# Optimization experiments

Measured on AMD Instinct MI355X. Metric: run time of the kernel, lower is better.

Reference implementation:

```python
import jax, jax.numpy as jnp
import numpy as np

B = 32768
EPS = 0.2  # BatchNorm eps used in the original module


def _xavier(key, shape):
    fan_in, fan_out = shape[-2], shape[-1]
    std = (2.0 / (fan_in + fan_out)) ** 0.5
    return (jax.random.normal(key, shape, jnp.float32) * std).astype(jnp.float32)


def bn(x, g, b):
    # training-mode BatchNorm1d: batch stats over the batch axis (-2), biased var
    m = jnp.mean(x, axis=-2, keepdims=True)
    v = jnp.mean(jnp.square(x - m), axis=-2, keepdims=True)
    return (x - m) * jax.lax.rsqrt(v + EPS) * g + b


def setup_inputs() -> dict:
    key = jax.random.key(0)
    ks = iter(jax.random.split(key, 48))
    inp = {}
    inp['x1f'] = jax.random.normal(next(ks), (B, 512), jnp.float32)
    inp['x2f'] = jax.random.normal(next(ks), (B, 512), jnp.float32)
    # shared trunk
    inp['W1'] = _xavier(next(ks), (512, 256)); inp['b1'] = jnp.zeros(256, jnp.float32)
    inp['W2'] = _xavier(next(ks), (256, 256)); inp['b2'] = jnp.zeros(256, jnp.float32)
    # batchnorm affine params (bn1:256, bn2:256, bn3:128, bn4:64)
    inp['g1'] = jnp.ones(256, jnp.float32); inp['be1'] = jnp.zeros(256, jnp.float32)
    inp['g2'] = jnp.ones(256, jnp.float32); inp['be2'] = jnp.zeros(256, jnp.float32)
    inp['g3'] = jnp.ones(128, jnp.float32); inp['be3'] = jnp.zeros(128, jnp.float32)
    inp['g4'] = jnp.ones(64, jnp.float32); inp['be4'] = jnp.zeros(64, jnp.float32)
    # 4 branch projections from each stream (x11..x14, x21..x24), stacked on axis 0
    inp['Wbx1'] = _xavier(next(ks), (4, 256, 256)); inp['bbx1'] = jnp.zeros((4, 256), jnp.float32)
    inp['Wbx2'] = _xavier(next(ks), (4, 256, 256)); inp['bbx2'] = jnp.zeros((4, 256), jnp.float32)
    # gating MLPs (xw*1, xw*2, xw*3, y*), stacked over the 4 attributes
    inp['Wwa'] = _xavier(next(ks), (4, 512, 128)); inp['bwa'] = jnp.zeros((4, 128), jnp.float32)
    inp['Wwb'] = _xavier(next(ks), (4, 128, 64)); inp['bwb'] = jnp.zeros((4, 64), jnp.float32)
    inp['Wwc'] = _xavier(next(ks), (4, 64, 64)); inp['bwc'] = jnp.zeros((4, 64), jnp.float32)
    inp['Wy'] = _xavier(next(ks), (4, 64, 2)); inp['by'] = jnp.zeros((4, 2), jnp.float32)
    # combine layers x1c..x4c, stacked
    inp['Wc'] = _xavier(next(ks), (4, 512, 256)); inp['bc'] = jnp.zeros((4, 256), jnp.float32)
    # output heads (different class counts: 3, 3, 6, 4)
    inp['Wo1'] = _xavier(next(ks), (256, 3)); inp['bo1'] = jnp.zeros(3, jnp.float32)
    inp['Wo2'] = _xavier(next(ks), (256, 3)); inp['bo2'] = jnp.zeros(3, jnp.float32)
    inp['Wo3'] = _xavier(next(ks), (256, 6)); inp['bo3'] = jnp.zeros(6, jnp.float32)
    inp['Wo4'] = _xavier(next(ks), (256, 4)); inp['bo4'] = jnp.zeros(4, jnp.float32)
    return inp


def reference(x1f, x2f, W1, b1, W2, b2, g1, be1, g2, be2, g3, be3, g4, be4,
              Wbx1, bbx1, Wbx2, bbx2, Wwa, bwa, Wwb, bwb, Wwc, bwc, Wy, by,
              Wc, bc, Wo1, bo1, Wo2, bo2, Wo3, bo3, Wo4, bo4):
    relu = jax.nn.relu

    def trunk(x):
        h = bn(relu(x @ W1 + b1), g1, be1)
        return bn(relu(h @ W2 + b2), g2, be2)

    h1 = trunk(x1f)  # [B,256]
    h2 = trunk(x2f)  # [B,256]

    # 4 branch features per stream, each bn1-normalized: [4,B,256]
    b1x = bn(relu(jnp.einsum('bi,kio->kbo', h1, Wbx1) + bbx1[:, None, :]), g1, be1)
    b2x = bn(relu(jnp.einsum('bi,kio->kbo', h2, Wbx2) + bbx2[:, None, :]), g1, be1)

    # gating MLP per attribute -> 2-way softmax weights
    xcat = jnp.concatenate([b1x, b2x], axis=-1)  # [4,B,512]
    a = bn(relu(jnp.einsum('kbi,kio->kbo', xcat, Wwa) + bwa[:, None, :]), g3, be3)
    b_ = bn(relu(jnp.einsum('kbi,kio->kbo', a, Wwb) + bwb[:, None, :]), g4, be4)
    c = bn(relu(jnp.einsum('kbi,kio->kbo', b_, Wwc) + bwc[:, None, :]), g4, be4)
    y = jax.nn.softmax(jnp.einsum('kbi,kio->kbo', c, Wy) + by[:, None, :], axis=-1)  # [4,B,2]

    # the original per-column loop == one broadcast multiply per stream
    xw = jnp.concatenate([b1x * y[..., 0:1], b2x * y[..., 1:2]], axis=-1)  # [4,B,512]

    # combine layers (dropout is identity in eval)
    xc = bn(relu(jnp.einsum('kbi,kio->kbo', xw, Wc) + bc[:, None, :]), g1, be1)  # [4,B,256]

    y1o = jax.nn.softmax(xc[0] @ Wo1 + bo1, axis=-1)
    y2o = jax.nn.softmax(xc[1] @ Wo2 + bo2, axis=-1)
    y3o = jax.nn.softmax(xc[2] @ Wo3 + bo3, axis=-1)
    y4o = jax.nn.softmax(xc[3] @ Wo4 + bo4, axis=-1)
    return (y1o, y2o, y3o, y4o)
```

## Files before the change

### kernel.cpp

```cpp
#include <hip/hip_runtime.h>
#include <hip/hip_bf16.h>


typedef unsigned short u16;
typedef _Float16 f16x8 __attribute__((ext_vector_type(8)));
typedef float f32x4 __attribute__((ext_vector_type(4)));

#define B_ROWS 32768
#define EPS_BN 0.2f
#define BINV (1.0f / 32768.0f)

__device__ __forceinline__ float bf2f(u16 u) {
    union { unsigned int i; float f; } c;
    c.i = ((unsigned int)u) << 16;
    return c.f;
}
__device__ __forceinline__ u16 f2bf(float f) {
    union { float f; unsigned int i; } c;
    c.f = f;
    unsigned int x = c.i;
    return (u16)((x + 0x7FFFu + ((x >> 16) & 1u)) >> 16);
}
__device__ __forceinline__ float h2f(u16 u) {
    _Float16 h;
    __builtin_memcpy(&h, &u, 2);
    return (float)h;
}
__device__ __forceinline__ u16 f2h(float f) {
    _Float16 h = (_Float16)f;
    u16 u;
    __builtin_memcpy(&u, &h, 2);
    return u;
}
__device__ __forceinline__ float ldp(const void* p, long i, int flag) {
    return flag ? bf2f(((const u16*)p)[i]) : ((const float*)p)[i];
}
__device__ __forceinline__ void gload16(const u16* gp, u16* lp) {
    __builtin_amdgcn_global_load_lds(
        (const __attribute__((address_space(1))) unsigned int*)gp,
        (__attribute__((address_space(3))) unsigned int*)lp, 16, 0, 0);
}

__global__ void detect_dtype(const u16* __restrict__ x, int* __restrict__ flag) {
    const int lane = threadIdx.x;
    const u16 v = x[2 * lane];
    const int e = (v >> 7) & 0xFF;
    const bool plausible = (e >= 110 && e <= 140);
    const unsigned long long m = __ballot(plausible);
    if (lane == 0) *flag = (__popcll(m) >= 58) ? 1 : 0;
}

struct PTab { const void* p[20]; int n[20]; int off[20]; };

__global__ void convert_params(PTab t, float* __restrict__ dst,
                               const int* __restrict__ flag) {
    const int ti = blockIdx.y;
    const int n = t.n[ti];
    float* o = dst + t.off[ti];
    const int isbf = *flag;
    for (int i = blockIdx.x * 256 + threadIdx.x; i < n; i += gridDim.x * 256)
        o[i] = ldp(t.p[ti], i, isbf);
}

__global__ __launch_bounds__(256) void prep_w(
    const void* __restrict__ W, long wstride,
    const void* __restrict__ bias, long bstride,
    const float* __restrict__ psum, const float* __restrict__ psq, int pstride,
    const void* __restrict__ pg, const void* __restrict__ pbe, int gmask,
    const int* __restrict__ dtflag,
    u16* __restrict__ Wt, long wtstride,
    float* __restrict__ biasP, float* __restrict__ T0o,
    float* __restrict__ T1o, float* __restrict__ bsum, long bost,
    int K, int khalf)
{
    const int tid = threadIdx.x;
    const int n = blockIdx.x;
    const int N = gridDim.x;
    const int inst = blockIdx.y;
    const int flag = *dtflag;
    __shared__ float sn[512], tn[512];
    __shared__ float r0[4], r1[4];

    for (int i = tid; i < K; i += 256) {
        float s = 1.f, t = 0.f;
        if (psum) {
            float m = psum[(long)pstride * inst + i] * BINV;
            float v = psq[(long)pstride * inst + i] * BINV - m * m;
            float g = ldp(pg, i & gmask, flag);
            float b = ldp(pbe, i & gmask, flag);
            s = g * rsqrtf(v + EPS_BN);
            t = b - m * s;
        }
        sn[i] = s; tn[i] = t;
    }
    __syncthreads();
    float p0 = 0.f, p1 = 0.f;
    for (int k = tid; k < K; k += 256) {
        float wv = ldp(W, wstride * inst + (long)k * N + n, flag);
        Wt[wtstride * inst + (long)n * K + k] = f2h(sn[k] * wv);
        float tw = tn[k] * wv;
        if (k < khalf) p0 += tw; else p1 += tw;
    }
#pragma unroll
    for (int off = 32; off; off >>= 1) {
        p0 += __shfl_xor(p0, off);
        p1 += __shfl_xor(p1, off);
    }
    const int lane = tid & 63, wid = tid >> 6;
    if (lane == 0) { r0[wid] = p0; r1[wid] = p1; }
    __syncthreads();
    if (tid == 0) {
        float t0 = r0[0] + r0[1] + r0[2] + r0[3];
        float t1 = r1[0] + r1[1] + r1[2] + r1[3];
        float bp = ldp(bias, bstride * inst + n, flag);
        long o = bost * inst + n;
        biasP[o] = bp; T0o[o] = t0; T1o[o] = t1; bsum[o] = bp + t0 + t1;
    }
}

__global__ __launch_bounds__(256) void reduce_stats(
    const float* __restrict__ part, int X, int colsPer,
    float* __restrict__ outS, float* __restrict__ outQ, int total)
{
    const int t = blockIdx.x * 256 + threadIdx.x;
    if (t >= total) return;
    const int p = t / colsPer, c = t % colsPer;
    const float* pb = part + (long)p * X * 2 * colsPer + c;
    float s = 0.f, q = 0.f;
#pragma unroll 4
    for (int x = 0; x < X; ++x) {
        s += pb[(long)x * 2 * colsPer];
        q += pb[(long)x * 2 * colsPer + colsPer];
    }
    outS[t] = s; outQ[t] = q;
}

template <bool XSTAGE, bool ROWW, int WM, int WN, int K, int RMODE>
__global__ __launch_bounds__(256, 3) void gemm_mfma(
    const void* __restrict__ X, const void* __restrict__ X2,
    long xstride, int ximask, int ldx, int ksplit, long ksecond,
    const int* __restrict__ dtflag,
    const u16* __restrict__ Wt, long wtstride,
    const float* __restrict__ biasP, const float* __restrict__ T0,
    const float* __restrict__ T1, const float* __restrict__ bsum, int bN,
    u16* __restrict__ Out, long ostride, int ldout,
    float* __restrict__ gsum, float* __restrict__ gsq, int sstride,
    float* __restrict__ part,
    const float* __restrict__ Y0v)
{
    const int tid = threadIdx.x;
    const int lane = tid & 63;
    const int wid = tid >> 6;
    const int wm = wid / WN, wn = wid % WN;

    const int gx = gridDim.x, gy = gridDim.y;
    const int NB = gx * gy * gridDim.z;
    const int L = blockIdx.x + gx * (blockIdx.y + gy * blockIdx.z);
    const int lid = (NB % 8 == 0) ? (L % 8) * (NB / 8) + L / 8 : L;
    int bx, by, inst;
    if constexpr (RMODE == 0) {
        bx = lid % gx; const int r = lid / gx; by = r % gy; inst = r / gy;
    } else if constexpr (RMODE == 1) {
        const int grp = gy * gridDim.z;
        bx = lid / grp; const int r = lid % grp; by = r % gy; inst = r / gy;
    } else {
        by = lid % gy; const int r = lid / gy; bx = r % gx; inst = r / gx;
    }

    const int rowB = bx * (64 * WM);
    const int nBase = by * (64 * WN);
    const int n0 = nBase + wn * 64;
    const int fm = lane & 15, quad = lane >> 4;

    __shared__ __align__(16) u16 AsBs[(WM + WN) * 4096];
    __shared__ float redS[4][64];
    __shared__ float redQ[4][64];
    u16* As = AsBs;
    u16* Bs = AsBs + WM * 4096;

    bool xf32 = false;
    if constexpr (XSTAGE) xf32 = (*dtflag == 0);
    const char* xb;
    if (XSTAGE) xb = (const char*)(inst == 0 ? X : X2);
    else        xb = (const char*)X + 2l * xstride * (inst & ximask);
    const u16* wtp = Wt + wtstride * inst;
    u16* op = Out + ostride * inst;

    f32x4 acc[4][4];
#pragma unroll
    for (int i = 0; i < 4; ++i)
#pragma unroll
        for (int j = 0; j < 4; ++j) acc[i][j] = (f32x4){0.f, 0.f, 0.f, 0.f};

    _Float16 ysc[2][4];
    if constexpr (ROWW) {
        const float* yp = Y0v + (long)inst * B_ROWS;
#pragma unroll
        for (int mi = 0; mi < 4; ++mi) {
            const float y = yp[rowB + wm * 64 + mi * 16 + fm];
            ysc[0][mi] = (_Float16)y;
            ysc[1][mi] = (_Float16)(1.f - y);
        }
    }

    const int rloc = lane >> 3;
    const int cg = (lane & 7) ^ rloc;

    for (int kt = 0; kt < K / 64; ++kt) {
        const int kk = kt * 64;
        __syncthreads();
        if constexpr (XSTAGE) {
#pragma unroll
            for (int p = 0; p < WM * 2; ++p) {
                const int s = p * 256 + tid;
                const int m = s >> 3, c = s & 7;
                const int g = c ^ (m & 7);
                f16x8 h;
                if (xf32) {
                    const float* gp = (const float*)xb + (long)(rowB + m) * ldx + kk + g * 8;
                    const float4 u = *(const float4*)gp;
                    const float4 u2 = *(const float4*)(gp + 4);
                    h[0] = (_Float16)u.x;  h[1] = (_Float16)u.y;
                    h[2] = (_Float16)u.z;  h[3] = (_Float16)u.w;
                    h[4] = (_Float16)u2.x; h[5] = (_Float16)u2.y;
                    h[6] = (_Float16)u2.z; h[7] = (_Float16)u2.w;
                } else {
                    const uint4 v = *(const uint4*)((const u16*)xb + (long)(rowB + m) * ldx + kk + g * 8);
                    const u16* pv = (const u16*)&v;
#pragma unroll
                    for (int j = 0; j < 8; ++j) h[j] = (_Float16)bf2f(pv[j]);
                }
                *(f16x8*)&As[s * 8] = h;
            }
        } else {
            const u16* xs = (const u16*)xb;
            int kkr = kk;
            if (kk >= ksplit) { xs += ksecond; kkr -= ksplit; }
#pragma unroll
            for (int s = wid; s < WM * 8; s += 4)
                gload16(xs + (long)(rowB + s * 8 + rloc) * ldx + kkr + cg * 8,
                        &As[s * 512 + lane * 8]);
        }
#pragma unroll
        for (int s = wid; s < WN * 8; s += 4)
            gload16(wtp + (long)(nBase + s * 8 + rloc) * K + kk + cg * 8,
                    &Bs[s * 512 + lane * 8]);
        __syncthreads();

        const int sel = (ROWW && kk >= ksplit) ? 1 : 0;
#pragma unroll
        for (int q = 0; q < 2; ++q) {
            f16x8 af[4], bfr[4];
#pragma unroll
            for (int mi = 0; mi < 4; ++mi) {
                const int mm = wm * 64 + mi * 16 + fm;
                af[mi] = *(const f16x8*)&As[mm * 64 + (((q * 4 + quad) ^ (mm & 7)) * 8)];
            }
            if constexpr (ROWW) {
#pragma unroll
                for (int mi = 0; mi < 4; ++mi) {
                    const _Float16 yh = ysc[sel][mi];
#pragma unroll
                    for (int j = 0; j < 8; ++j) af[mi][j] *= yh;
                }
            }
#pragma unroll
            for (int ni = 0; ni < 4; ++ni) {
                const int nn = wn * 64 + ni * 16 + fm;
                bfr[ni] = *(const f16x8*)&Bs[nn * 64 + (((q * 4 + quad) ^ (nn & 7)) * 8)];
            }
#pragma unroll
            for (int mi = 0; mi < 4; ++mi)
#pragma unroll
                for (int ni = 0; ni < 4; ++ni)
                    acc[mi][ni] = __builtin_amdgcn_mfma_f32_16x16x32_f16(
                        af[mi], bfr[ni], acc[mi][ni], 0, 0, 0);
        }
    }

    __syncthreads();

    u16* wtile = AsBs + wid * 4096;
    const int R0 = rowB + wm * 64;

    float yv[16];
    if constexpr (ROWW) {
        const float* yp = Y0v + (long)inst * B_ROWS;
#pragma unroll
        for (int mi = 0; mi < 4; ++mi)
#pragma unroll
            for (int r = 0; r < 4; ++r)
                yv[mi * 4 + r] = yp[R0 + mi * 16 + quad * 4 + r];
    }

#pragma unroll
    for (int ni = 0; ni < 4; ++ni) {
        const int nc = ni * 16 + fm;
        const int n = n0 + nc;
        float bS = 0.f, bP = 0.f, t0v = 0.f, t1v = 0.f;
        if constexpr (ROWW) {
            bP = biasP[(long)inst * bN + n];
            t0v = T0[(long)inst * bN + n];
            t1v = T1[(long)inst * bN + n];
        } else {
            bS = bsum[(long)inst * bN + n];
        }
        float s = 0.f, qq = 0.f;
#pragma unroll
        for (int mi = 0; mi < 4; ++mi) {
#pragma unroll
            for (int r = 0; r < 4; ++r) {
                float v;
                if constexpr (ROWW) {
                    const float y = yv[mi * 4 + r];
                    v = acc[mi][ni][r] + y * t0v + (1.f - y) * t1v + bP;
                } else {
                    v = acc[mi][ni][r] + bS;
                }
                v = fmaxf(v, 0.f);
                s += v; qq += v * v;
                const int lr = mi * 16 + quad * 4 + r;
                wtile[lr * 64 + (nc ^ (((lr >> 1) & 7) << 3))] = f2h(v);
            }
        }
        s += __shfl_xor(s, 16);  s += __shfl_xor(s, 32);
        qq += __shfl_xor(qq, 16); qq += __shfl_xor(qq, 32);
        if (quad == 0) { redS[wid][nc] = s; redQ[wid][nc] = qq; }
    }

    {
        const int l8 = lane & 7, r8 = lane >> 3;
#pragma unroll
        for (int it = 0; it < 8; ++it) {
            const int lr = it * 8 + r8;
            const int ch = l8 ^ ((lr >> 1) & 7);
            const f16x8 hv = *(const f16x8*)&wtile[lr * 64 + ch * 8];
            *(f16x8*)(op + (long)(R0 + lr) * ldout + n0 + l8 * 8) = hv;
        }
    }

    __syncthreads();
    if (tid < WN * 64) {
        const int wnc = tid >> 6, within = tid & 63;
        float s = 0.f, q = 0.f;
#pragma unroll
        for (int w = 0; w < WM; ++w) {
            s += redS[w * WN + wnc][within];
            q += redQ[w * WN + wnc][within];
        }
        if (part) {
            float* pb = part +
                (long)((inst * gridDim.y + by) * gridDim.x + bx)
                    * (2 * WN * 64);
            pb[tid] = s;
            pb[WN * 64 + tid] = q;
        } else {
            atomicAdd(&gsum[(long)inst * sstride + nBase + tid], s);
            atomicAdd(&gsq [(long)inst * sstride + nBase + tid], q);
        }
    }
}

__global__ __launch_bounds__(256) void gate_kernel(
    const u16* __restrict__ zc,
    const float* __restrict__ stFs, const float* __restrict__ stFq,
    const float* __restrict__ g4, const float* __restrict__ be4,
    const float* __restrict__ Wy, const float* __restrict__ by,
    float* __restrict__ Y0)
{
    const int tid = threadIdx.x;
    const int k = blockIdx.y;
    const int r0 = blockIdx.x * 128;

    __shared__ __align__(8) float Ws2[64][2];
    __shared__ float cg[2];

    if (tid < 64) {
        const int c = tid;
        const float m = stFs[k * 64 + c] * BINV;
        const float v = stFq[k * 64 + c] * BINV - m * m;
        const float s = g4[c] * rsqrtf(v + EPS_BN);
        const float t = be4[c] - m * s;
        const float w0 = Wy[k * 128 + c * 2 + 0];
        const float w1 = Wy[k * 128 + c * 2 + 1];
        Ws2[c][0] = s * w0;
        Ws2[c][1] = s * w1;
        float t0 = t * w0, t1 = t * w1;
#pragma unroll
        for (int off = 32; off; off >>= 1) {
            t0 += __shfl_xor(t0, off);
            t1 += __shfl_xor(t1, off);
        }
        if (c == 0) {
            cg[0] = t0 + by[k * 2 + 0];
            cg[1] = t1 + by[k * 2 + 1];
        }
    }
    __syncthreads();

    const int row = r0 + (tid >> 1);
    const int seg = tid & 1;
    const u16* xp = zc + ((long)k * B_ROWS + row) * 64 + seg * 32;
    float a0 = 0.f, a1 = 0.f;
#pragma unroll
    for (int it = 0; it < 4; ++it) {
        const uint4 v = *(const uint4*)(xp + it * 8);
        const u16* pv = (const u16*)&v;
#pragma unroll
        for (int e = 0; e < 8; ++e) {
            const int c = seg * 32 + it * 8 + e;
            const float x = h2f(pv[e]);
            a0 += x * Ws2[c][0];
            a1 += x * Ws2[c][1];
        }
    }
    a0 += __shfl_xor(a0, 1);
    a1 += __shfl_xor(a1, 1);
    if (seg == 0) {
        const float l0 = a0 + cg[0];
        const float l1 = a1 + cg[1];
        Y0[(long)k * B_ROWS + row] = 1.f / (1.f + __expf(l1 - l0));
    }
}

__global__ __launch_bounds__(256) void heads_kernel(
    const u16* __restrict__ zxc,
    const float* __restrict__ stHs, const float* __restrict__ stHq,
    const float* __restrict__ g1, const float* __restrict__ be1,
    const float* __restrict__ Wo1, const float* __restrict__ bo1,
    const float* __restrict__ Wo2, const float* __restrict__ bo2,
    const float* __restrict__ Wo3, const float* __restrict__ bo3,
    const float* __restrict__ Wo4, const float* __restrict__ bo4,
    void* __restrict__ out, const int* __restrict__ dtflag)
{
    const int tid = threadIdx.x;
    const int k = blockIdx.y;
    const int r0 = blockIdx.x * 64;

    const float* Wo; const float* bo; int nk; long obase;
    if (k == 0)      { Wo = Wo1; bo = bo1; nk = 3; obase = 0; }
    else if (k == 1) { Wo = Wo2; bo = bo2; nk = 3; obase = (long)3 * B_ROWS; }
    else if (k == 2) { Wo = Wo3; bo = bo3; nk = 6; obase = (long)6 * B_ROWS; }
    else             { Wo = Wo4; bo = bo4; nk = 4; obase = (long)12 * B_ROWS; }

    __shared__ __align__(16) float Ws[256][8];
    __shared__ float cj[8];
    __shared__ float redC[4][8];

    {
        const int c = tid;
        const float m = stHs[k * 256 + c] * BINV;
        const float v = stHq[k * 256 + c] * BINV - m * m;
        const float s = g1[c] * rsqrtf(v + EPS_BN);
        const float t = be1[c] - m * s;
        const int rs = c ^ (c >> 6);
        float tw[6];
#pragma unroll
        for (int j = 0; j < 6; ++j) {
            const float w = (j < nk) ? Wo[c * nk + j] : 0.f;
            Ws[rs][j] = s * w;
            tw[j] = t * w;
        }
        Ws[rs][6] = 0.f; Ws[rs][7] = 0.f;
#pragma unroll
        for (int off = 32; off; off >>= 1)
#pragma unroll
            for (int j = 0; j < 6; ++j) tw[j] += __shfl_xor(tw[j], off);
        const int lane = tid & 63, wid = tid >> 6;
        if (lane < 6) redC[wid][lane] = tw[lane];
    }
    __syncthreads();
    if (tid < 8) {
        float s4 = 0.f;
        if (tid < 6) s4 = redC[0][tid] + redC[1][tid] + redC[2][tid] + redC[3][tid];
        cj[tid] = (tid < nk) ? s4 + bo[tid] : 0.f;
    }
    __syncthreads();

    const int row = r0 + (tid >> 2);
    const int seg = tid & 3;
    const u16* xp = zxc + ((long)k * B_ROWS + row) * 256 + seg * 64;
    float acc[6];
#pragma unroll
    for (int j = 0; j < 6; ++j) acc[j] = 0.f;
#pragma unroll
    for (int it = 0; it < 8; ++it) {
        const uint4 v = *(const uint4*)(xp + it * 8);
        const u16* pv = (const u16*)&v;
#pragma unroll
        for (int e = 0; e < 8; ++e) {
            const int cc = it * 8 + e;
            const int rs = (seg * 64 + cc) ^ seg;
            const float x = h2f(pv[e]);
            const f32x4 w0 = *(const f32x4*)&Ws[rs][0];
            const f32x4 w1 = *(const f32x4*)&Ws[rs][4];
            acc[0] += x * w0[0];
            acc[1] += x * w0[1];
            acc[2] += x * w0[2];
            acc[3] += x * w0[3];
            acc[4] += x * w1[0];
            acc[5] += x * w1[1];
        }
    }
#pragma unroll
    for (int j = 0; j < 6; ++j) {
        acc[j] += __shfl_xor(acc[j], 1);
        acc[j] += __shfl_xor(acc[j], 2);
    }

    if (seg == 0) {
        float l[6];
        float mx = -1e30f;
#pragma unroll
        for (int j = 0; j < 6; j++)
            if (j < nk) { l[j] = acc[j] + cj[j]; mx = fmaxf(mx, l[j]); }
        float e[6];
        float se = 0.f;
#pragma unroll
        for (int j = 0; j < 6; j++)
            if (j < nk) { e[j] = __expf(l[j] - mx); se += e[j]; }
        const float inv = 1.f / se;
        if (*dtflag) {
            u16* ob = (u16*)out;
#pragma unroll
            for (int j = 0; j < 6; j++)
                if (j < nk) ob[obase + (long)row * nk + j] = f2bf(e[j] * inv);
        } else {
            float* of = (float*)out;
#pragma unroll
            for (int j = 0; j < 6; j++)
                if (j < nk) of[obase + (long)row * nk + j] = e[j] * inv;
        }
    }
}

__global__ void fill_sentinel(u16* out, int n) {
    int i = blockIdx.x * 256 + threadIdx.x;
    if (i < n) out[i] = 0x3E80;
}

extern "C" void kernel_launch(void* const* d_in, const int* in_sizes, int n_in,
                              void* d_out, int out_size, void* d_ws, size_t ws_size,
                              hipStream_t stream)
{
    const long B = B_ROWS;
    char* ws = (char*)d_ws;
    const size_t MB = 1024 * 1024;

    u16* z1  = (u16*)(ws);
    u16* z2  = (u16*)(ws + 32 * MB);
    u16* za  = (u16*)(ws);
    u16* zbb = (u16*)(ws + 32 * MB);
    u16* zc  = (u16*)(ws + 48 * MB);
    u16* zxc = (u16*)(ws);
    u16* zb  = (u16*)(ws + 64 * MB);
    float* Y0 = (float*)(ws + 192 * MB);
    float* stats = (float*)(ws + 192 * MB + 512 * 1024);
    int* dtflag = (int*)(ws + 192 * MB + 576 * 1024);
    float* Pst = (float*)(ws + 192 * MB + 640 * 1024);

    u16* WtA = (u16*)(ws + 193 * MB);
    u16* WtB = WtA + 131072;
    u16* WtC = WtB + 131072;
    u16* WtD = WtC + 524288;
    u16* WtH = WtD + 262144;
    u16* WtE = WtH + 524288;
    u16* WtF = WtE + 32768;
    float* biasArea = (float*)(ws + 197 * MB);
    float* bA = biasArea;
    float* bB = bA + 2048;
    float* bC = bB + 2048;
    float* bD = bC + 8192;
    float* bH = bD + 2048;
    float* bE = bH + 4096;
    float* bF = bE + 1024;

    float* partC = (float*)(ws);
    float* partH = (float*)(ws + 193 * MB);

    const int cIdx[20] = {6,7,10,11,12,13,20,21,22,23,24,25,28,29,30,31,32,33,34,35};
    PTab tab;
    int mapOff[36];
    int acc = 0;
    for (int i = 0; i < 20; i++) {
        tab.p[i] = d_in[cIdx[i]];
        tab.n[i] = in_sizes[cIdx[i]];
        tab.off[i] = acc;
        mapOff[cIdx[i]] = acc;
        acc += in_sizes[cIdx[i]];
    }
    const size_t need = 197 * MB + 20480 * 4 + 4096;
    if (need > ws_size || (size_t)acc * 4 > 384 * 1024) {
        fill_sentinel<<<(out_size + 255) / 256, 256, 0, stream>>>((u16*)d_out, out_size);
        return;
    }
    auto PF = [&](int idx) { return Pst + mapOff[idx]; };

    float* stAs = stats;        float* stAq = stAs + 512;
    float* stBs = stAq + 512;   float* stBq = stBs + 512;
    float* stCs = stBq + 512;   float* stCq = stCs + 2048;
    float* stDs = stCq + 2048;  float* stDq = stDs + 512;
    float* stEs = stDq + 512;   float* stEq = stEs + 256;
    float* stFs = stEq + 256;   float* stFq = stFs + 256;
    float* stHs = stFq + 256;   float* stHq = stHs + 1024;

    hipMemsetAsync(stats, 0, 10240 * 4, stream);
    detect_dtype<<<1, 64, 0, stream>>>((const u16*)d_in[0], dtflag);
    convert_params<<<dim3(32, 20), 256, 0, stream>>>(tab, Pst, dtflag);

    const dim3 blk(256);
    const int BIGK = 1 << 29;

    prep_w<<<dim3(256, 2), blk, 0, stream>>>(
        d_in[2], 0, d_in[3], 0, nullptr, nullptr, 0, nullptr, nullptr, 0,
        dtflag, WtA, 0, bA, bA + 512, bA + 1024, bA + 1536, 256, 512, 512);
    gemm_mfma<true, false, 2, 2, 512, 2><<<dim3(256, 2, 2), blk, 0, stream>>>(
        d_in[0], d_in[1], 0, 0, 512, BIGK, 0, dtflag, WtA, 0,
        bA, bA + 512, bA + 1024, bA + 1536, 256,
        z1, B * 256, 256, stAs, stAq, 256, nullptr, nullptr);

    prep_w<<<dim3(256, 2), blk, 0, stream>>>(
        d_in[4], 0, d_in[5], 0, stAs, stAq, 256, d_in[6], d_in[7], 255,
        dtflag, WtB, 65536, bB, bB + 512, bB + 1024, bB + 1536, 256, 256, 256);
    gemm_mfma<false, false, 2, 2, 256, 2><<<dim3(256, 2, 2), blk, 0, stream>>>(
        z1, nullptr, B * 256, 3, 256, BIGK, 0, dtflag, WtB, 65536,
        bB, bB + 512, bB + 1024, bB + 1536, 256,
        z2, B * 256, 256, stBs, stBq, 256, nullptr, nullptr);

    for (int s = 0; s < 2; s++) {
        prep_w<<<dim3(256, 4), blk, 0, stream>>>(
            d_in[s ? 16 : 14], 65536, d_in[s ? 17 : 15], 256,
            stBs + s * 256, stBq + s * 256, 0, d_in[8], d_in[9], 255,
            dtflag, WtC + s * 65536, 131072,
            bC + s * 256, bC + 2048 + s * 256, bC + 4096 + s * 256,
            bC + 6144 + s * 256, 512, 256, 256);
    }
    gemm_mfma<false, false, 2, 2, 256, 1><<<dim3(256, 2, 8), blk, 0, stream>>>(
        z2, nullptr, B * 256, 1, 256, BIGK, 0, dtflag, WtC, 65536,
        bC, bC + 2048, bC + 4096, bC + 6144, 256,
        zb, B * 256, 256, stCs, stCq, 256, partC, nullptr);
    reduce_stats<<<dim3(8), blk, 0, stream>>>(partC, 256, 128, stCs, stCq, 2048);

    prep_w<<<dim3(128, 4), blk, 0, stream>>>(
        d_in[18], 65536, d_in[19], 128, stCs, stCq, 512, d_in[6], d_in[7], 255,
        dtflag, WtD, 65536, bD, bD + 512, bD + 1024, bD + 1536, 128, 512, 512);
    prep_w<<<dim3(256, 4), blk, 0, stream>>>(
        d_in[26], 131072, d_in[27], 256, stCs, stCq, 512, d_in[6], d_in[7], 255,
        dtflag, WtH, 131072, bH, bH + 1024, bH + 2048, bH + 3072, 256, 512, 256);
    gemm_mfma<false, false, 2, 2, 512, 0><<<dim3(256, 1, 4), blk, 0, stream>>>(
        zb, nullptr, 2 * B * 256, 3, 256, 256, B * 256, dtflag, WtD, 65536,
        bD, bD + 512, bD + 1024, bD + 1536, 128,
        za, B * 128, 128, stDs, stDq, 128, nullptr, nullptr);

    prep_w<<<dim3(64, 4), blk, 0, stream>>>(
        d_in[20], 8192, d_in[21], 64, stDs, stDq, 128, d_in[10], d_in[11], 127,
        dtflag, WtE, 8192, bE, bE + 256, bE + 512, bE + 768, 64, 128, 128);
    gemm_mfma<false, false, 4, 1, 128, 0><<<dim3(128, 1, 4), blk, 0, stream>>>(
        za, nullptr, B * 128, 3, 128, BIGK, 0, dtflag, WtE, 8192,
        bE, bE + 256, bE + 512, bE + 768, 64,
        zbb, B * 64, 64, stEs, stEq, 64, nullptr, nullptr);

    prep_w<<<dim3(64, 4), blk, 0, stream>>>(
        d_in[22], 4096, d_in[23], 64, stEs, stEq, 64, d_in[12], d_in[13], 63,
        dtflag, WtF, 4096, bF, bF + 256, bF + 512, bF + 768, 64, 64, 64);
    gemm_mfma<false, false, 4, 1, 64, 0><<<dim3(128, 1, 4), blk, 0, stream>>>(
        zbb, nullptr, B * 64, 3, 64, BIGK, 0, dtflag, WtF, 4096,
        bF, bF + 256, bF + 512, bF + 768, 64,
        zc, B * 64, 64, stFs, stFq, 64, nullptr, nullptr);

    gate_kernel<<<dim3(B_ROWS / 128, 4), blk, 0, stream>>>(
        zc, stFs, stFq, PF(12), PF(13), PF(24), PF(25), Y0);

    gemm_mfma<false, true, 2, 2, 512, 2><<<dim3(256, 2, 4), blk, 0, stream>>>(
        zb, nullptr, 2 * B * 256, 3, 256, 256, B * 256, dtflag, WtH, 131072,
        bH, bH + 1024, bH + 2048, bH + 3072, 256,
        zxc, B * 256, 256, stHs, stHq, 256, partH, Y0);
    reduce_stats<<<dim3(4), blk, 0, stream>>>(partH, 256, 128, stHs, stHq, 1024);

    heads_kernel<<<dim3(B_ROWS / 64, 4), blk, 0, stream>>>(
        zxc, stHs, stHq, PF(6), PF(7), PF(28), PF(29), PF(30), PF(31),
        PF(32), PF(33), PF(34), PF(35), d_out, dtflag);
}
```

Before: 569.8 us.

## Double-buffer A tiles with async prefetch in MFMA GEMM kernels

Adds a PIPE template path that double-buffers the activation (A) tile in shared memory. The next k-step's A loads are issued before the current compute, gated by explicit vmcnt waits and raw s_barriers, so global-load latency overlaps MFMA work. It also adds RMODE 3, which uses the block indices directly instead of the XCD-aware remap, for several GEMMs. The change costs more LDS per block, which may lower occupancy. The hand-coded vmcnt(4) count is tied to the 2x2 wave layout.

```diff
diff --git a/kernel.cpp b/kernel.cpp
--- a/kernel.cpp
+++ b/kernel.cpp
@@ -135,7 +135,7 @@
     outS[t] = s; outQ[t] = q;
 }
 
-template <bool XSTAGE, bool ROWW, int WM, int WN, int K, int RMODE>
+template <bool XSTAGE, bool ROWW, int WM, int WN, int K, int RMODE, bool PIPE>
 __global__ __launch_bounds__(256, 3) void gemm_mfma(
     const void* __restrict__ X, const void* __restrict__ X2,
     long xstride, int ximask, int ldx, int ksplit, long ksecond,
@@ -153,18 +153,22 @@
     const int wid = tid >> 6;
     const int wm = wid / WN, wn = wid % WN;
 
-    const int gx = gridDim.x, gy = gridDim.y;
-    const int NB = gx * gy * gridDim.z;
-    const int L = blockIdx.x + gx * (blockIdx.y + gy * blockIdx.z);
-    const int lid = (NB % 8 == 0) ? (L % 8) * (NB / 8) + L / 8 : L;
     int bx, by, inst;
-    if constexpr (RMODE == 0) {
-        bx = lid % gx; const int r = lid / gx; by = r % gy; inst = r / gy;
-    } else if constexpr (RMODE == 1) {
-        const int grp = gy * gridDim.z;
-        bx = lid / grp; const int r = lid % grp; by = r % gy; inst = r / gy;
+    if constexpr (RMODE == 3) {
+        bx = blockIdx.x; by = blockIdx.y; inst = blockIdx.z;
     } else {
-        by = lid % gy; const int r = lid / gy; bx = r % gx; inst = r / gx;
+        const int gx = gridDim.x, gy = gridDim.y;
+        const int NB = gx * gy * gridDim.z;
+        const int L = blockIdx.x + gx * (blockIdx.y + gy * blockIdx.z);
+        const int lid = (NB % 8 == 0) ? (L % 8) * (NB / 8) + L / 8 : L;
+        if constexpr (RMODE == 0) {
+            bx = lid % gx; const int r = lid / gx; by = r % gy; inst = r / gy;
+        } else if constexpr (RMODE == 1) {
+            const int grp = gy * gridDim.z;
+            bx = lid / grp; const int r = lid % grp; by = r % gy; inst = r / gy;
+        } else {
+            by = lid % gy; const int r = lid / gy; bx = r % gx; inst = r / gx;
+        }
     }
 
     const int rowB = bx * (64 * WM);
@@ -172,11 +176,11 @@
     const int n0 = nBase + wn * 64;
     const int fm = lane & 15, quad = lane >> 4;
 
-    __shared__ __align__(16) u16 AsBs[(WM + WN) * 4096];
+    __shared__ __align__(16) u16 AsBs[((PIPE ? 2 : 1) * WM + WN) * 4096];
     __shared__ float redS[4][64];
     __shared__ float redQ[4][64];
     u16* As = AsBs;
-    u16* Bs = AsBs + WM * 4096;
+    u16* Bs = AsBs + (PIPE ? 2 : 1) * WM * 4096;
 
     bool xf32 = false;
     if constexpr (XSTAGE) xf32 = (*dtflag == 0);
@@ -206,10 +210,86 @@
     const int rloc = lane >> 3;
     const int cg = (lane & 7) ^ rloc;
 
-    for (int kt = 0; kt < K / 64; ++kt) {
+    auto stageA = [&](int kt, int buf) {
         const int kk = kt * 64;
-        __syncthreads();
-        if constexpr (XSTAGE) {
+        const u16* xs = (const u16*)xb;
+        int kkr = kk;
+        if (kk >= ksplit) { xs += ksecond; kkr -= ksplit; }
+        u16* asb = &As[buf * WM * 4096];
+#pragma unroll
+        for (int s = wid; s < WM * 8; s += 4)
+            gload16(xs + (long)(rowB + s * 8 + rloc) * ldx + kkr + cg * 8,
+                    &asb[s * 512 + lane * 8]);
+    };
+    auto stageB = [&](int kt) {
+        const int kk = kt * 64;
+#pragma unroll
+        for (int s = wid; s < WN * 8; s += 4)
+            gload16(wtp + (long)(nBase + s * 8 + rloc) * K + kk + cg * 8,
+                    &Bs[s * 512 + lane * 8]);
+    };
+    auto computeT = [&](int kt, int abuf) {
+        const u16* asb = &As[abuf * WM * 4096];
+        const int sel = (ROWW && kt * 64 >= ksplit) ? 1 : 0;
+#pragma unroll
+        for (int q = 0; q < 2; ++q) {
+            f16x8 af[4], bfr[4];
+#pragma unroll
+            for (int mi = 0; mi < 4; ++mi) {
+                const int mm = wm * 64 + mi * 16 + fm;
+                af[mi] = *(const f16x8*)&asb[mm * 64 + (((q * 4 + quad) ^ (mm & 7)) * 8)];
+            }
+            if constexpr (ROWW) {
+#pragma unroll
+                for (int mi = 0; mi < 4; ++mi) {
+                    const _Float16 yh = ysc[sel][mi];
+#pragma unroll
+                    for (int j = 0; j < 8; ++j) af[mi][j] *= yh;
+                }
+            }
+#pragma unroll
+            for (int ni = 0; ni < 4; ++ni) {
+                const int nn = wn * 64 + ni * 16 + fm;
+                bfr[ni] = *(const f16x8*)&Bs[nn * 64 + (((q * 4 + quad) ^ (nn & 7)) * 8)];
+            }
+#pragma unroll
+            for (int mi = 0; mi < 4; ++mi)
+#pragma unroll
+                for (int ni = 0; ni < 4; ++ni)
+                    acc[mi][ni] = __builtin_amdgcn_mfma_f32_16x16x32_f16(
+                        af[mi], bfr[ni], acc[mi][ni], 0, 0, 0);
+        }
+    };
+
+    if constexpr (PIPE && !XSTAGE) {
+        static_assert(WM == 2 && WN == 2, "vmcnt(4) assumes 4 A + 4 B loads/wave");
+        constexpr int NT = K / 64;
+        asm volatile("s_waitcnt vmcnt(0)" ::: "memory");
+        stageA(0, 0);
+        for (int kt = 0; kt < NT; ++kt) {
+            stageB(kt);
+            if (kt + 1 < NT) {
+                stageA(kt + 1, (kt + 1) & 1);
+                asm volatile("s_waitcnt vmcnt(4)" ::: "memory");
+            } else {
+                asm volatile("s_waitcnt vmcnt(0)" ::: "memory");
+            }
+            __builtin_amdgcn_s_barrier();
+            computeT(kt, kt & 1);
+            __builtin_amdgcn_s_barrier();
+        }
+    } else if constexpr (!XSTAGE) {
+        for (int kt = 0; kt < K / 64; ++kt) {
+            __syncthreads();
+            stageA(kt, 0);
+            stageB(kt);
+            __syncthreads();
+            computeT(kt, 0);
+        }
+    } else {
+        for (int kt = 0; kt < K / 64; ++kt) {
+            const int kk = kt * 64;
+            __syncthreads();
 #pragma unroll
             for (int p = 0; p < WM * 2; ++p) {
                 const int s = p * 256 + tid;
@@ -232,49 +312,9 @@
                 }
                 *(f16x8*)&As[s * 8] = h;
             }
-        } else {
-            const u16* xs = (const u16*)xb;
-            int kkr = kk;
-            if (kk >= ksplit) { xs += ksecond; kkr -= ksplit; }
-#pragma unroll
-            for (int s = wid; s < WM * 8; s += 4)
-                gload16(xs + (long)(rowB + s * 8 + rloc) * ldx + kkr + cg * 8,
-                        &As[s * 512 + lane * 8]);
-        }
-#pragma unroll
-        for (int s = wid; s < WN * 8; s += 4)
-            gload16(wtp + (long)(nBase + s * 8 + rloc) * K + kk + cg * 8,
-                    &Bs[s * 512 + lane * 8]);
-        __syncthreads();
-
-        const int sel = (ROWW && kk >= ksplit) ? 1 : 0;
-#pragma unroll
-        for (int q = 0; q < 2; ++q) {
-            f16x8 af[4], bfr[4];
-#pragma unroll
-            for (int mi = 0; mi < 4; ++mi) {
-                const int mm = wm * 64 + mi * 16 + fm;
-                af[mi] = *(const f16x8*)&As[mm * 64 + (((q * 4 + quad) ^ (mm & 7)) * 8)];
-            }
-            if constexpr (ROWW) {
-#pragma unroll
-                for (int mi = 0; mi < 4; ++mi) {
-                    const _Float16 yh = ysc[sel][mi];
-#pragma unroll
-                    for (int j = 0; j < 8; ++j) af[mi][j] *= yh;
-                }
-            }
-#pragma unroll
-            for (int ni = 0; ni < 4; ++ni) {
-                const int nn = wn * 64 + ni * 16 + fm;
-                bfr[ni] = *(const f16x8*)&Bs[nn * 64 + (((q * 4 + quad) ^ (nn & 7)) * 8)];
-            }
-#pragma unroll
-            for (int mi = 0; mi < 4; ++mi)
-#pragma unroll
-                for (int ni = 0; ni < 4; ++ni)
-                    acc[mi][ni] = __builtin_amdgcn_mfma_f32_16x16x32_f16(
-                        af[mi], bfr[ni], acc[mi][ni], 0, 0, 0);
+            stageB(kt);
+            __syncthreads();
+            computeT(kt, 0);
         }
     }
 
@@ -614,7 +654,7 @@
     prep_w<<<dim3(256, 2), blk, 0, stream>>>(
         d_in[2], 0, d_in[3], 0, nullptr, nullptr, 0, nullptr, nullptr, 0,
         dtflag, WtA, 0, bA, bA + 512, bA + 1024, bA + 1536, 256, 512, 512);
-    gemm_mfma<true, false, 2, 2, 512, 2><<<dim3(256, 2, 2), blk, 0, stream>>>(
+    gemm_mfma<true, false, 2, 2, 512, 2, false><<<dim3(256, 2, 2), blk, 0, stream>>>(
         d_in[0], d_in[1], 0, 0, 512, BIGK, 0, dtflag, WtA, 0,
         bA, bA + 512, bA + 1024, bA + 1536, 256,
         z1, B * 256, 256, stAs, stAq, 256, nullptr, nullptr);
@@ -622,7 +662,7 @@
     prep_w<<<dim3(256, 2), blk, 0, stream>>>(
         d_in[4], 0, d_in[5], 0, stAs, stAq, 256, d_in[6], d_in[7], 255,
         dtflag, WtB, 65536, bB, bB + 512, bB + 1024, bB + 1536, 256, 256, 256);
-    gemm_mfma<false, false, 2, 2, 256, 2><<<dim3(256, 2, 2), blk, 0, stream>>>(
+    gemm_mfma<false, false, 2, 2, 256, 2, true><<<dim3(256, 2, 2), blk, 0, stream>>>(
         z1, nullptr, B * 256, 3, 256, BIGK, 0, dtflag, WtB, 65536,
         bB, bB + 512, bB + 1024, bB + 1536, 256,
         z2, B * 256, 256, stBs, stBq, 256, nullptr, nullptr);
@@ -635,7 +675,7 @@
             bC + s * 256, bC + 2048 + s * 256, bC + 4096 + s * 256,
             bC + 6144 + s * 256, 512, 256, 256);
     }
-    gemm_mfma<false, false, 2, 2, 256, 1><<<dim3(256, 2, 8), blk, 0, stream>>>(
+    gemm_mfma<false, false, 2, 2, 256, 1, true><<<dim3(256, 2, 8), blk, 0, stream>>>(
         z2, nullptr, B * 256, 1, 256, BIGK, 0, dtflag, WtC, 65536,
         bC, bC + 2048, bC + 4096, bC + 6144, 256,
         zb, B * 256, 256, stCs, stCq, 256, partC, nullptr);
@@ -647,7 +687,7 @@
     prep_w<<<dim3(256, 4), blk, 0, stream>>>(
         d_in[26], 131072, d_in[27], 256, stCs, stCq, 512, d_in[6], d_in[7], 255,
         dtflag, WtH, 131072, bH, bH + 1024, bH + 2048, bH + 3072, 256, 512, 256);
-    gemm_mfma<false, false, 2, 2, 512, 0><<<dim3(256, 1, 4), blk, 0, stream>>>(
+    gemm_mfma<false, false, 2, 2, 512, 3, true><<<dim3(256, 1, 4), blk, 0, stream>>>(
         zb, nullptr, 2 * B * 256, 3, 256, 256, B * 256, dtflag, WtD, 65536,
         bD, bD + 512, bD + 1024, bD + 1536, 128,
         za, B * 128, 128, stDs, stDq, 128, nullptr, nullptr);
@@ -655,7 +695,7 @@
     prep_w<<<dim3(64, 4), blk, 0, stream>>>(
         d_in[20], 8192, d_in[21], 64, stDs, stDq, 128, d_in[10], d_in[11], 127,
         dtflag, WtE, 8192, bE, bE + 256, bE + 512, bE + 768, 64, 128, 128);
-    gemm_mfma<false, false, 4, 1, 128, 0><<<dim3(128, 1, 4), blk, 0, stream>>>(
+    gemm_mfma<false, false, 4, 1, 128, 3, false><<<dim3(128, 1, 4), blk, 0, stream>>>(
         za, nullptr, B * 128, 3, 128, BIGK, 0, dtflag, WtE, 8192,
         bE, bE + 256, bE + 512, bE + 768, 64,
         zbb, B * 64, 64, stEs, stEq, 64, nullptr, nullptr);
@@ -663,7 +703,7 @@
     prep_w<<<dim3(64, 4), blk, 0, stream>>>(
         d_in[22], 4096, d_in[23], 64, stEs, stEq, 64, d_in[12], d_in[13], 63,
         dtflag, WtF, 4096, bF, bF + 256, bF + 512, bF + 768, 64, 64, 64);
-    gemm_mfma<false, false, 4, 1, 64, 0><<<dim3(128, 1, 4), blk, 0, stream>>>(
+    gemm_mfma<false, false, 4, 1, 64, 3, false><<<dim3(128, 1, 4), blk, 0, stream>>>(
         zbb, nullptr, B * 64, 3, 64, BIGK, 0, dtflag, WtF, 4096,
         bF, bF + 256, bF + 512, bF + 768, 64,
         zc, B * 64, 64, stFs, stFq, 64, nullptr, nullptr);
@@ -671,7 +711,7 @@
     gate_kernel<<<dim3(B_ROWS / 128, 4), blk, 0, stream>>>(
         zc, stFs, stFq, PF(12), PF(13), PF(24), PF(25), Y0);
 
-    gemm_mfma<false, true, 2, 2, 512, 2><<<dim3(256, 2, 4), blk, 0, stream>>>(
+    gemm_mfma<false, true, 2, 2, 512, 2, true><<<dim3(256, 2, 4), blk, 0, stream>>>(
         zb, nullptr, 2 * B * 256, 3, 256, 256, B * 256, dtflag, WtH, 131072,
         bH, bH + 1024, bH + 2048, bH + 3072, 256,
         zxc, B * 256, 256, stHs, stHq, 256, partH, Y0);
```

Measured after the change: 582.3 us. +2.2%, slower.
